# Optimization experiments

Measured on AMD Instinct MI355X. Metric: run time of the kernel, lower is better.

## Reference

```python
import jax, jax.numpy as jnp
import numpy as np

DIM = 1536
NH = 12
HD = DIM // NH  # 128
F_, H_, W_ = 16, 16, 16
L = F_ * H_ * W_  # 4096


def _precompute_freqs(dim, max_positions, base=10000.0):
    # [max_positions, dim//2] angles
    half = dim // 2
    inv = 1.0 / base ** (np.arange(0, half * 2, 2, dtype=np.float32) / (half * 2))
    pos = np.arange(max_positions, dtype=np.float32)
    return pos[:, None] * inv[None, :]


def _get_3d_freqs(head_dim, F, H, W, base=10000.0):
    half_hd = head_dim // 2
    n_t = max(1, head_dim // 4 // 2)
    n_h = max(1, head_dim * 3 // 8 // 2)
    n_w = half_hd - n_t - n_h
    ft = _precompute_freqs(n_t * 2, F, base)  # [F, n_t]
    fh = _precompute_freqs(n_h * 2, H, base)  # [H, n_h]
    fw = _precompute_freqs(n_w * 2, W, base)  # [W, n_w]
    f_idx = np.broadcast_to(ft[:, None, None, :], (F, H, W, n_t))
    h_idx = np.broadcast_to(fh[None, :, None, :], (F, H, W, n_h))
    w_idx = np.broadcast_to(fw[None, None, :, :], (F, H, W, n_w))
    return np.concatenate([f_idx, h_idx, w_idx], axis=-1).reshape(F * H * W, half_hd)


def setup_inputs() -> dict:
    key = jax.random.key(0)
    ks = jax.random.split(key, 9)
    s = 1.0 / np.sqrt(DIM)
    x = jax.random.normal(ks[0], (1, L, DIM), dtype=jnp.float32)
    freqs = jnp.asarray(_get_3d_freqs(HD, F_, H_, W_), dtype=jnp.float32)
    Wq = jax.random.normal(ks[1], (DIM, DIM), dtype=jnp.float32) * s
    bq = jax.random.normal(ks[2], (DIM,), dtype=jnp.float32) * 0.01
    Wk = jax.random.normal(ks[3], (DIM, DIM), dtype=jnp.float32) * s
    bk = jax.random.normal(ks[4], (DIM,), dtype=jnp.float32) * 0.01
    Wv = jax.random.normal(ks[5], (DIM, DIM), dtype=jnp.float32) * s
    bv = jax.random.normal(ks[6], (DIM,), dtype=jnp.float32) * 0.01
    Wo = jax.random.normal(ks[7], (DIM, DIM), dtype=jnp.float32) * s
    bo = jax.random.normal(ks[8], (DIM,), dtype=jnp.float32) * 0.01
    return {"x": x, "freqs": freqs, "Wq": Wq, "bq": bq, "Wk": Wk, "bk": bk,
            "Wv": Wv, "bv": bv, "Wo": Wo, "bo": bo}


def _apply_rotary(t, cos_v, sin_v):
    # t: [B, Nh, L, Hd]; cos_v/sin_v: [L, Hd//2]
    B, Nh, Lq, Hd = t.shape
    t2 = t.reshape(B, Nh, Lq, Hd // 2, 2)
    x0, x1 = t2[..., 0], t2[..., 1]
    r0 = x0 * cos_v - x1 * sin_v
    r1 = x0 * sin_v + x1 * cos_v
    return jnp.stack([r0, r1], axis=-1).reshape(B, Nh, Lq, Hd)


def reference(x, freqs, Wq, bq, Wk, bk, Wv, bv, Wo, bo):
    B, Lq, D = x.shape
    Nh, Hd = NH, D // NH
    q = (x @ Wq + bq).reshape(B, Lq, Nh, Hd).transpose(0, 2, 1, 3)
    k = (x @ Wk + bk).reshape(B, Lq, Nh, Hd).transpose(0, 2, 1, 3)
    v = (x @ Wv + bv).reshape(B, Lq, Nh, Hd).transpose(0, 2, 1, 3)
    cos_v = jnp.cos(freqs)  # [L, Hd//2]
    sin_v = jnp.sin(freqs)
    q = _apply_rotary(q, cos_v, sin_v)
    k = _apply_rotary(k, cos_v, sin_v)
    scale = 1.0 / jnp.sqrt(jnp.asarray(Hd, dtype=x.dtype))
    scores = jnp.einsum('bhqd,bhkd->bhqk', q, k) * scale
    attn = jax.nn.softmax(scores, axis=-1)
    out = jnp.einsum('bhqk,bhkd->bhqd', attn, v)
    out = out.transpose(0, 2, 1, 3).reshape(B, Lq, D)
    return out @ Wo + bo
```

## Files before the change

kernel.cpp:

```cpp
#include <hip/hip_runtime.h>

#define DIM 1536
#define NH  12
#define HD  128
#define SEQ 4096

typedef unsigned short u16;
typedef unsigned int   u32;
typedef __attribute__((ext_vector_type(8))) short bf16x8;
typedef __attribute__((ext_vector_type(4))) float f32x4;
typedef __attribute__((ext_vector_type(16))) float f32x16;

static __device__ __forceinline__ u16 f2bf(float f) {
    u32 u = __float_as_uint(f);
    u32 r = u + 0x7FFFu + ((u >> 16) & 1u);
    return (u16)(r >> 16);
}
static __device__ __forceinline__ float bf2f(u16 h) {
    return __uint_as_float(((u32)h) << 16);
}
static __device__ __forceinline__ u32 pack2(float a, float b) {
    return (u32)f2bf(a) | ((u32)f2bf(b) << 16);
}

#define GLL(g, s) __builtin_amdgcn_global_load_lds( \
    (const __attribute__((address_space(1))) void*)(g), \
    (__attribute__((address_space(3))) void*)(s), 16, 0, 0)

__global__ __launch_bounds__(256) void k_cvt_x(const float* __restrict__ x, u16* __restrict__ xb) {
    int gid = blockIdx.x * 256 + threadIdx.x;
    const float4* p = (const float4*)x + (size_t)gid * 2;
    float4 a = p[0], b = p[1];
    uint4 o;
    o.x = pack2(a.x, a.y); o.y = pack2(a.z, a.w);
    o.z = pack2(b.x, b.y); o.w = pack2(b.z, b.w);
    *(uint4*)(xb + (size_t)gid * 8) = o;
}

__global__ __launch_bounds__(256) void k_transpose_w(const float* __restrict__ Wq, const float* __restrict__ Wk,
                                                     const float* __restrict__ Wv, const float* __restrict__ Wo,
                                                     u16* __restrict__ wqkv, u16* __restrict__ wot) {
    __shared__ float tile[32][33];
    int z = blockIdx.z;
    const float* W = z == 0 ? Wq : z == 1 ? Wk : z == 2 ? Wv : Wo;
    u16* out = z < 3 ? (wqkv + (size_t)z * DIM * DIM) : wot;
    int tx = threadIdx.x, ty = threadIdx.y;
    int c0 = blockIdx.x * 32, r0 = blockIdx.y * 32;
#pragma unroll
    for (int i = 0; i < 4; i++)
        tile[ty + i * 8][tx] = W[(size_t)(r0 + ty + i * 8) * DIM + c0 + tx];
    __syncthreads();
#pragma unroll
    for (int i = 0; i < 4; i++)
        out[(size_t)(c0 + ty + i * 8) * DIM + r0 + tx] = f2bf(tile[tx][ty + i * 8]);
}

__global__ __launch_bounds__(256) void k_tr_v(const u16* __restrict__ vb, u16* __restrict__ vt) {
    __shared__ u16 tile[32][33];
    int h = blockIdx.z;
    int l0 = blockIdx.x * 32, d0 = blockIdx.y * 32;
    int tx = threadIdx.x, ty = threadIdx.y;
    const u16* src = vb + (size_t)h * SEQ * HD;
    u16* dst = vt + (size_t)h * HD * SEQ;
#pragma unroll
    for (int i = 0; i < 4; i++)
        tile[ty + i * 8][tx] = src[(size_t)(l0 + ty + i * 8) * HD + d0 + tx];
    __syncthreads();
#pragma unroll
    for (int i = 0; i < 4; i++)
        dst[(size_t)(d0 + ty + i * 8) * SEQ + l0 + tx] = tile[tx][ty + i * 8];
}

__global__ __launch_bounds__(256) void k_prep(const float* __restrict__ fr, const float* __restrict__ bq,
                                              const float* __restrict__ bk, const float* __restrict__ bv,
                                              float2* __restrict__ cs, float* __restrict__ bqkv) {
    int gid = blockIdx.x * 256 + threadIdx.x;
    float f = fr[gid];
    cs[gid] = make_float2(cosf(f), sinf(f));
    if (gid < 3 * DIM)
        bqkv[gid] = gid < DIM ? bq[gid] : gid < 2 * DIM ? bk[gid - DIM] : bv[gid - 2 * DIM];
}

__global__ __launch_bounds__(256) void k_gemm(const u16* __restrict__ A, const u16* __restrict__ B,
                                              const float* __restrict__ bias, int Kdim, int mode,
                                              u16* __restrict__ qo, u16* __restrict__ ko,
                                              u16* __restrict__ vo, float* __restrict__ outf) {
    __shared__ u16 As[128 * 32];
    __shared__ u16 Bs[128 * 32];
    const int tid = threadIdx.x;
    const int w = tid >> 6, l = tid & 63;
    const int wr = w >> 1, wc = w & 1;
    const int lr = l & 15, lg = l >> 4;
    int nwg = gridDim.x * gridDim.y;
    int bid = blockIdx.y * gridDim.x + blockIdx.x;
    int swz = (bid & 7) * (nwg >> 3) + (bid >> 3);
    const int m0 = (swz / gridDim.x) * 128, n0 = (swz % gridDim.x) * 128;
    f32x4 acc[4][4] = {};

    const int srow = l >> 2;
    const int scol = (((l & 3) * 16) ^ (((l >> 2) & 3) << 4)) >> 1;

    for (int kt = 0; kt < Kdim; kt += 32) {
        __syncthreads();
#pragma unroll
        for (int c2 = 0; c2 < 2; ++c2) {
            int c = w * 2 + c2;
            int row = c * 16 + srow;
            GLL(A + (size_t)(m0 + row) * Kdim + kt + scol, As + c * 512);
            GLL(B + (size_t)(n0 + row) * Kdim + kt + scol, Bs + c * 512);
        }
        __syncthreads();
        bf16x8 af[4], bg[4];
#pragma unroll
        for (int i = 0; i < 4; i++) {
            int co = (lg * 8) ^ ((lr & 3) << 3);
            af[i] = *(const bf16x8*)(As + (wr * 64 + i * 16 + lr) * 32 + co);
            bg[i] = *(const bf16x8*)(Bs + (wc * 64 + i * 16 + lr) * 32 + co);
        }
#pragma unroll
        for (int i = 0; i < 4; i++)
#pragma unroll
            for (int j = 0; j < 4; j++)
                acc[i][j] = __builtin_amdgcn_mfma_f32_16x16x32_bf16(af[i], bg[j], acc[i][j], 0, 0, 0);
    }

#pragma unroll
    for (int j = 0; j < 4; j++) {
        int gc = n0 + wc * 64 + j * 16 + lr;
        float bb = bias[gc];
#pragma unroll
        for (int i = 0; i < 4; i++) {
            int gr0 = m0 + wr * 64 + i * 16 + lg * 4;
            if (mode == 0) {
                int t = gc / DIM;
                int rr = gc % DIM;
                int hh = rr >> 7, hd = rr & 127;
                u16* dst = t == 0 ? qo : t == 1 ? ko : vo;
                size_t base = (size_t)hh * SEQ * HD + hd;
#pragma unroll
                for (int r = 0; r < 4; r++)
                    dst[base + (size_t)(gr0 + r) * HD] = f2bf(acc[i][j][r] + bb);
            } else {
#pragma unroll
                for (int r = 0; r < 4; r++)
                    outf[(size_t)(gr0 + r) * DIM + gc] = acc[i][j][r] + bb;
            }
        }
    }
}

__global__ __launch_bounds__(256) void k_rope(u16* __restrict__ qb, u16* __restrict__ kb,
                                              const float2* __restrict__ cs) {
    int gid = blockIdx.x * 256 + threadIdx.x;
    const int T = NH * SEQ * 64;
    u16* buf = gid < T ? qb : kb;
    int r = gid < T ? gid : gid - T;
    int hh = r / (SEQ * 64);
    int rr = r % (SEQ * 64);
    int ll = rr >> 6, ii = rr & 63;
    size_t off = ((size_t)hh * SEQ + ll) * HD + 2 * ii;
    u32 pk = *(const u32*)(buf + off);
    float x0 = bf2f((u16)(pk & 0xFFFFu)), x1 = bf2f((u16)(pk >> 16));
    float2 c = cs[ll * 64 + ii];
    float r0 = x0 * c.x - x1 * c.y;
    float r1 = x0 * c.y + x1 * c.x;
    *(u32*)(buf + off) = pack2(r0, r1);
}

__global__ __launch_bounds__(256, 3) void k_attn(const u16* __restrict__ qb, const u16* __restrict__ kbuf,
                                                 const u16* __restrict__ vt, u16* __restrict__ attnb) {
    __shared__ u16 Ks[64 * 128];
    __shared__ u16 Vs[128 * 64];
    __shared__ float MB[128][18];
    const int tid = threadIdx.x;
    const int w = tid >> 6, l = tid & 63;
    const int qh = w & 1, kh = w >> 1;
    const int g = l >> 5, qlane = l & 31;
    const int lr = l & 15, lg = l >> 4;
    int bid = blockIdx.x;
    int gw = (bid & 7) * 96 + (bid >> 3);
    const int h = gw >> 6;
    const int q0 = (gw & 63) << 6;
    const size_t hb = (size_t)h * SEQ * HD;
    constexpr float SCL2 = 0.08838834764831845f * 1.4426950408889634f;
    constexpr float THR = 5.0f;

    const int vrow8 = l >> 3;
    const int vc0 = (((l & 7) * 16) ^ (vrow8 << 4)) >> 1;

    bf16x8 qf[8];
    {
        const u16* qp = qb + hb + (size_t)(q0 + qh * 32 + qlane) * HD + g * 8;
#pragma unroll
        for (int s = 0; s < 8; s++)
            qf[s] = *(const bf16x8*)(qp + s * 16);
    }
    f32x16 O[4] = {};
    float m_run = -1e30f, lsum = 0.f;

    const int krow = kh * 32 + qlane;
    const int ksw = (krow & 7) << 4;
    const int vswl = (qlane & 7) << 4;

    for (int kt = 0; kt < SEQ; kt += 64) {
        __syncthreads();
#pragma unroll
        for (int c = 0; c < 4; c++) {
            int cc = w * 4 + c;
            int key = cc * 4 + lg;
            int kd0 = ((lr * 16) ^ ((key & 7) << 4)) >> 1;
            GLL(kbuf + hb + (size_t)(kt + key) * HD + kd0, Ks + cc * 512);
            int dd = cc * 8 + vrow8;
            GLL(vt + hb + (size_t)dd * SEQ + kt + vc0, Vs + cc * 512);
        }
        __syncthreads();

        f32x16 ST = {};
        const u16* Kp = Ks + krow * 128;
#pragma unroll
        for (int s = 0; s < 8; s++) {
            bf16x8 kf = *(const bf16x8*)(Kp + (((s * 32 + g * 16) ^ ksw) >> 1));
            ST = __builtin_amdgcn_mfma_f32_32x32x16_bf16(kf, qf[s], ST, 0, 0, 0);
        }

        float mx = ST[0];
#pragma unroll
        for (int r = 1; r < 16; r++) mx = fmaxf(mx, ST[r]);
        mx = fmaxf(mx, __shfl_xor(mx, 32));
        float mt = mx * SCL2;
        bool grow = mt > m_run + THR;
        float m_new = grow ? mt : m_run;
        if (__any(grow)) {
            float alpha = grow ? __builtin_amdgcn_exp2f(m_run - m_new) : 1.0f;
            lsum *= alpha;
            m_run = m_new;
#pragma unroll
            for (int db = 0; db < 4; db++)
#pragma unroll
                for (int r = 0; r < 16; r++) O[db][r] *= alpha;
        }
        float ps = 0.f;
#pragma unroll
        for (int r = 0; r < 16; r++) {
            float p = __builtin_amdgcn_exp2f(fmaf(ST[r], SCL2, -m_new));
            ST[r] = p; ps += p;
        }
        lsum += ps;

        u32 pw[2][4];
#pragma unroll
        for (int s2 = 0; s2 < 2; s2++) {
            int rb = s2 * 8;
            u32 a, b2, c2, d2;
            asm("v_cvt_pk_bf16_f32 %0, %1, %2" : "=v"(a)  : "v"(ST[rb + 0]), "v"(ST[rb + 1]));
            asm("v_cvt_pk_bf16_f32 %0, %1, %2" : "=v"(b2) : "v"(ST[rb + 2]), "v"(ST[rb + 3]));
            asm("v_cvt_pk_bf16_f32 %0, %1, %2" : "=v"(c2) : "v"(ST[rb + 4]), "v"(ST[rb + 5]));
            asm("v_cvt_pk_bf16_f32 %0, %1, %2" : "=v"(d2) : "v"(ST[rb + 6]), "v"(ST[rb + 7]));
            asm("v_permlane32_swap_b32 %0, %1" : "+v"(a), "+v"(c2));
            asm("v_permlane32_swap_b32 %0, %1" : "+v"(b2), "+v"(d2));
            pw[s2][0] = a; pw[s2][1] = b2; pw[s2][2] = c2; pw[s2][3] = d2;
        }

#pragma unroll
        for (int s2 = 0; s2 < 2; s2++) {
            union { u32 u[4]; bf16x8 v; } pf;
            pf.u[0] = pw[s2][0]; pf.u[1] = pw[s2][1]; pf.u[2] = pw[s2][2]; pf.u[3] = pw[s2][3];
            int kb2 = kh * 64 + s2 * 32 + g * 16;
#pragma unroll
            for (int db = 0; db < 4; db++) {
                int d = db * 32 + qlane;
                bf16x8 vf = *(const bf16x8*)(Vs + d * 64 + ((kb2 ^ vswl) >> 1));
                O[db] = __builtin_amdgcn_mfma_f32_32x32x16_bf16(vf, pf.v, O[db], 0, 0, 0);
            }
        }
    }

    lsum += __shfl_xor(lsum, 32);

    const int row = qh * 64 + l;
    u16* op = attnb + (size_t)(q0 + qh * 32 + qlane) * DIM + h * HD;
    __syncthreads();
    if (kh == 1) { MB[row][16] = m_run; MB[row][17] = lsum; }
    __syncthreads();
    float a0 = 0.f, a1 = 0.f;
    if (kh == 0) {
        float m1 = MB[row][16], l1 = MB[row][17];
        float mM = fmaxf(m_run, m1);
        a0 = __builtin_amdgcn_exp2f(m_run - mM);
        a1 = __builtin_amdgcn_exp2f(m1 - mM);
        float linv = 1.0f / (lsum * a0 + l1 * a1);
        a0 *= linv; a1 *= linv;
    }
#pragma unroll
    for (int db = 0; db < 4; db++) {
        __syncthreads();
        if (kh == 1) {
#pragma unroll
            for (int r = 0; r < 16; r++) MB[row][r] = O[db][r];
        }
        __syncthreads();
        if (kh == 0) {
#pragma unroll
            for (int r = 0; r < 16; r++) {
                int d = db * 32 + (r & 3) + 8 * (r >> 2) + 4 * g;
                op[d] = f2bf(O[db][r] * a0 + MB[row][r] * a1);
            }
        }
    }
}

extern "C" void kernel_launch(void* const* d_in, const int* in_sizes, int n_in,
                              void* d_out, int out_size, void* d_ws, size_t ws_size,
                              hipStream_t stream) {
    (void)in_sizes; (void)n_in; (void)out_size; (void)ws_size;
    const float* x  = (const float*)d_in[0];
    const float* fr = (const float*)d_in[1];
    const float* Wq = (const float*)d_in[2];
    const float* bq = (const float*)d_in[3];
    const float* Wk = (const float*)d_in[4];
    const float* bk = (const float*)d_in[5];
    const float* Wv = (const float*)d_in[6];
    const float* bv = (const float*)d_in[7];
    const float* Wo = (const float*)d_in[8];
    const float* bo = (const float*)d_in[9];
    float* out = (float*)d_out;

    char* ws = (char*)d_ws;
    size_t off = 0;
    auto alloc = [&](size_t b) { char* p = ws + off; off = (off + b + 255) & ~(size_t)255; return p; };
    u16*   xb    = (u16*)alloc((size_t)SEQ * DIM * 2);
    u16*   wqkv  = (u16*)alloc((size_t)3 * DIM * DIM * 2);
    u16*   wot   = (u16*)alloc((size_t)DIM * DIM * 2);
    float* bqkv  = (float*)alloc((size_t)3 * DIM * 4);
    u16*   qb    = (u16*)alloc((size_t)SEQ * DIM * 2);
    u16*   kb    = (u16*)alloc((size_t)SEQ * DIM * 2);
    u16*   vb    = (u16*)alloc((size_t)SEQ * DIM * 2);
    u16*   vtb   = (u16*)alloc((size_t)SEQ * DIM * 2);
    u16*   attnb = (u16*)alloc((size_t)SEQ * DIM * 2);
    float2* cs   = (float2*)alloc((size_t)SEQ * 64 * 8);

    k_cvt_x<<<3072, 256, 0, stream>>>(x, xb);
    k_transpose_w<<<dim3(48, 48, 4), dim3(32, 8), 0, stream>>>(Wq, Wk, Wv, Wo, wqkv, wot);
    k_prep<<<1024, 256, 0, stream>>>(fr, bq, bk, bv, cs, bqkv);
    k_gemm<<<dim3(36, 32), 256, 0, stream>>>(xb, wqkv, bqkv, DIM, 0, qb, kb, vb, nullptr);
    k_rope<<<24576, 256, 0, stream>>>(qb, kb, cs);
    k_tr_v<<<dim3(128, 4, 12), dim3(32, 8), 0, stream>>>(vb, vtb);
    k_attn<<<768, 256, 0, stream>>>(qb, kb, vtb, attnb);
    k_gemm<<<dim3(12, 32), 256, 0, stream>>>(attnb, wot, bo, DIM, 1, nullptr, nullptr, nullptr, out);
}
```

Measured before the change: 303.0 us.

## Double-buffer GEMM LDS tiles and vectorize RoPE kernel

The GEMM kernel now double-buffers its LDS tiles. It issues the global-to-LDS loads for the next K-step before computing on the current one, with a single barrier per iteration instead of two, so load latency can overlap with the MFMA work. Separately, the RoPE kernel now has each thread process 8 rotary pairs using 128-bit loads and stores, cutting the grid by 8x and reducing per-element indexing overhead. Double buffering doubles GEMM LDS use, which may lower occupancy.

```diff
diff --git a/kernel.cpp b/kernel.cpp
--- a/kernel.cpp
+++ b/kernel.cpp
@@ -85,8 +85,8 @@
                                               const float* __restrict__ bias, int Kdim, int mode,
                                               u16* __restrict__ qo, u16* __restrict__ ko,
                                               u16* __restrict__ vo, float* __restrict__ outf) {
-    __shared__ u16 As[128 * 32];
-    __shared__ u16 Bs[128 * 32];
+    __shared__ u16 As[2][128 * 32];
+    __shared__ u16 Bs[2][128 * 32];
     const int tid = threadIdx.x;
     const int w = tid >> 6, l = tid & 63;
     const int wr = w >> 1, wc = w & 1;
@@ -100,28 +100,44 @@
     const int srow = l >> 2;
     const int scol = (((l & 3) * 16) ^ (((l >> 2) & 3) << 4)) >> 1;
 
-    for (int kt = 0; kt < Kdim; kt += 32) {
-        __syncthreads();
-#pragma unroll
-        for (int c2 = 0; c2 < 2; ++c2) {
-            int c = w * 2 + c2;
-            int row = c * 16 + srow;
-            GLL(A + (size_t)(m0 + row) * Kdim + kt + scol, As + c * 512);
-            GLL(B + (size_t)(n0 + row) * Kdim + kt + scol, Bs + c * 512);
-        }
-        __syncthreads();
+    const int nk = Kdim >> 5;
+#pragma unroll
+    for (int c2 = 0; c2 < 2; ++c2) {
+        int c = w * 2 + c2;
+        int row = c * 16 + srow;
+        GLL(A + (size_t)(m0 + row) * Kdim + scol, As[0] + c * 512);
+        GLL(B + (size_t)(n0 + row) * Kdim + scol, Bs[0] + c * 512);
+    }
+    __syncthreads();
+
+    int cur = 0;
+    for (int t = 0; t < nk; ++t) {
+        if (t + 1 < nk) {
+            int kt = (t + 1) << 5;
+#pragma unroll
+            for (int c2 = 0; c2 < 2; ++c2) {
+                int c = w * 2 + c2;
+                int row = c * 16 + srow;
+                GLL(A + (size_t)(m0 + row) * Kdim + kt + scol, As[cur ^ 1] + c * 512);
+                GLL(B + (size_t)(n0 + row) * Kdim + kt + scol, Bs[cur ^ 1] + c * 512);
+            }
+        }
+        const u16* Ac = As[cur];
+        const u16* Bc = Bs[cur];
         bf16x8 af[4], bg[4];
 #pragma unroll
         for (int i = 0; i < 4; i++) {
             int co = (lg * 8) ^ ((lr & 3) << 3);
-            af[i] = *(const bf16x8*)(As + (wr * 64 + i * 16 + lr) * 32 + co);
-            bg[i] = *(const bf16x8*)(Bs + (wc * 64 + i * 16 + lr) * 32 + co);
+            af[i] = *(const bf16x8*)(Ac + (wr * 64 + i * 16 + lr) * 32 + co);
+            bg[i] = *(const bf16x8*)(Bc + (wc * 64 + i * 16 + lr) * 32 + co);
         }
 #pragma unroll
         for (int i = 0; i < 4; i++)
 #pragma unroll
             for (int j = 0; j < 4; j++)
                 acc[i][j] = __builtin_amdgcn_mfma_f32_16x16x32_bf16(af[i], bg[j], acc[i][j], 0, 0, 0);
+        __syncthreads();
+        cur ^= 1;
     }
 
 #pragma unroll
@@ -152,19 +168,28 @@
 __global__ __launch_bounds__(256) void k_rope(u16* __restrict__ qb, u16* __restrict__ kb,
                                               const float2* __restrict__ cs) {
     int gid = blockIdx.x * 256 + threadIdx.x;
-    const int T = NH * SEQ * 64;
+    const int T = NH * SEQ * 8;
     u16* buf = gid < T ? qb : kb;
     int r = gid < T ? gid : gid - T;
-    int hh = r / (SEQ * 64);
-    int rr = r % (SEQ * 64);
-    int ll = rr >> 6, ii = rr & 63;
-    size_t off = ((size_t)hh * SEQ + ll) * HD + 2 * ii;
-    u32 pk = *(const u32*)(buf + off);
-    float x0 = bf2f((u16)(pk & 0xFFFFu)), x1 = bf2f((u16)(pk >> 16));
-    float2 c = cs[ll * 64 + ii];
-    float r0 = x0 * c.x - x1 * c.y;
-    float r1 = x0 * c.y + x1 * c.x;
-    *(u32*)(buf + off) = pack2(r0, r1);
+    int hh = r / (SEQ * 8);
+    int rr = r % (SEQ * 8);
+    int ll = rr >> 3, i0 = (rr & 7) * 8;
+    size_t off = ((size_t)hh * SEQ + ll) * HD + 2 * i0;
+    uint4 pa = *(const uint4*)(buf + off);
+    uint4 pb = *(const uint4*)(buf + off + 8);
+    const float4* cp = (const float4*)(cs + (size_t)ll * 64 + i0);
+    float4 c0 = cp[0], c1 = cp[1], c2 = cp[2], c3 = cp[3];
+    auto rot = [](u32 pk, float cv, float sv) -> u32 {
+        float x0 = bf2f((u16)(pk & 0xFFFFu)), x1 = bf2f((u16)(pk >> 16));
+        return pack2(x0 * cv - x1 * sv, x0 * sv + x1 * cv);
+    };
+    uint4 oa, ob;
+    oa.x = rot(pa.x, c0.x, c0.y); oa.y = rot(pa.y, c0.z, c0.w);
+    oa.z = rot(pa.z, c1.x, c1.y); oa.w = rot(pa.w, c1.z, c1.w);
+    ob.x = rot(pb.x, c2.x, c2.y); ob.y = rot(pb.y, c2.z, c2.w);
+    ob.z = rot(pb.z, c3.x, c3.y); ob.w = rot(pb.w, c3.z, c3.w);
+    *(uint4*)(buf + off) = oa;
+    *(uint4*)(buf + off + 8) = ob;
 }
 
 __global__ __launch_bounds__(256, 3) void k_attn(const u16* __restrict__ qb, const u16* __restrict__ kbuf,
@@ -343,7 +368,7 @@
     k_transpose_w<<<dim3(48, 48, 4), dim3(32, 8), 0, stream>>>(Wq, Wk, Wv, Wo, wqkv, wot);
     k_prep<<<1024, 256, 0, stream>>>(fr, bq, bk, bv, cs, bqkv);
     k_gemm<<<dim3(36, 32), 256, 0, stream>>>(xb, wqkv, bqkv, DIM, 0, qb, kb, vb, nullptr);
-    k_rope<<<24576, 256, 0, stream>>>(qb, kb, cs);
+    k_rope<<<3072, 256, 0, stream>>>(qb, kb, cs);
     k_tr_v<<<dim3(128, 4, 12), dim3(32, 8), 0, stream>>>(vb, vtb);
     k_attn<<<768, 256, 0, stream>>>(qb, kb, vtb, attnb);
     k_gemm<<<dim3(12, 32), 256, 0, stream>>>(attnb, wot, bo, DIM, 1, nullptr, nullptr, nullptr, out);
```

After: 283.8 us. 6.3% less time.
